# Optimization experiments

Measured on AMD Instinct MI355X. Metric: run time of the kernel, lower is better.

## Reference

```python
import jax, jax.numpy as jnp
import numpy as np

B, H, N = 2, 4, 4096


def setup_inputs() -> dict:
    key = jax.random.key(0)
    ranking = jax.random.normal(key, (B, H, N, 1), dtype=jnp.float32)
    return {"ranking": ranking}


def reference(ranking):
    b_s, h, n = ranking.shape[:3]
    r = ranking[..., 0]  # [b, h, n]
    # stable descending argsort of ranking*100 (negate; jnp stable sort keeps tie order)
    sorted_idx = jnp.argsort(-r * 100.0, axis=2, stable=True)  # [b, h, n] int
    r_sort = jnp.take_along_axis(r, sorted_idx, axis=2)
    # rel_scaler = cumsum of ones = 1..n (no mask case)
    rel_scaler = jnp.cumsum(jnp.ones_like(r_sort), axis=2)
    rel_minus = jnp.cumsum(r_sort, axis=2)
    relative_ranking = rel_minus - rel_scaler * r_sort
    rel_scaler = jnp.maximum(rel_scaler - 1.0, 0.0)  # 0..n-1
    # Hrelu forward: hard ReLU (custom backward in torch; forward math is relu)
    rank = jax.nn.relu(relative_ranking)
    indicator = rel_scaler - rank
    indicator = jnp.where(indicator < 0, indicator + n, indicator)
    perm_value = jnp.exp(-indicator * 10.0)
    # sparse COO (bh, row, col) -> coalesce == scatter-add into dense [b*h, n, n]
    rows = rel_scaler.astype(jnp.int32).reshape(b_s * h, n)
    cols = sorted_idx.reshape(b_s * h, n).astype(jnp.int32)
    vals = perm_value.reshape(b_s * h, n)
    bh = jnp.arange(b_s * h, dtype=jnp.int32)[:, None]
    perm = jnp.zeros((b_s * h, n, n), jnp.float32).at[bh, rows, cols].add(vals)
    return perm
```

## Files before the change

kernel.cpp:

```cpp
#include <hip/hip_runtime.h>
#include <math.h>
#include <float.h>

#define N 4096
#define BH 8
#define THREADS 256
#define PARTS 32
#define EPB (N / PARTS)
#define CHUNK (N / THREADS)

__device__ __forceinline__ unsigned int desc_key(float r) {
    float k = r * 100.0f;
    unsigned int b = __float_as_uint(k);
    unsigned int asc = (b & 0x80000000u) ? ~b : (b | 0x80000000u);
    return ~asc;
}

__global__ __launch_bounds__(THREADS)
void rank_kernel(const float* __restrict__ ranking,
                 int* __restrict__ cols,
                 float* __restrict__ rsort) {
    __shared__ unsigned int keys[N];
    __shared__ unsigned short partial[THREADS];

    const int bh   = blockIdx.x / PARTS;
    const int part = blockIdx.x % PARTS;
    const float* r = ranking + (size_t)bh * N;

    for (int i = threadIdx.x; i < N; i += THREADS)
        keys[i] = desc_key(r[i]);
    __syncthreads();

    const int e_local = threadIdx.x & (EPB - 1);
    const int half    = threadIdx.x >> 7;
    const int e       = part * EPB + e_local;
    const unsigned int mykey = keys[e];

    int cnt = 0;
    const uint4* k4 = (const uint4*)keys;
    const int k4_begin = half * (N / 8);
    #pragma unroll 4
    for (int k = k4_begin; k < k4_begin + N / 8; ++k) {
        uint4 kk = k4[k];
        int kb = k * 4;
        cnt += (kk.x < mykey) || (kk.x == mykey && (kb + 0) < e);
        cnt += (kk.y < mykey) || (kk.y == mykey && (kb + 1) < e);
        cnt += (kk.z < mykey) || (kk.z == mykey && (kb + 2) < e);
        cnt += (kk.w < mykey) || (kk.w == mykey && (kb + 3) < e);
    }
    partial[threadIdx.x] = (unsigned short)cnt;
    __syncthreads();

    if (half == 0) {
        int rank = cnt + (int)partial[threadIdx.x + 128];
        size_t o = (size_t)bh * N + rank;
        cols[o]  = e;
        rsort[o] = r[e];
    }
}

__global__ __launch_bounds__(THREADS)
void scan_kernel(const float* __restrict__ rsort,
                 float* __restrict__ vals) {
    __shared__ double chunk_sums[THREADS];

    const int bh  = blockIdx.x;
    const int tid = threadIdx.x;
    const float* rs = rsort + (size_t)bh * N;
    const int base = tid * CHUNK;

    float  v[CHUNK];
    double local[CHUNK];
    const float4* f4 = (const float4*)(rs + base);
    #pragma unroll
    for (int q = 0; q < CHUNK / 4; ++q) {
        float4 w = f4[q];
        v[q * 4 + 0] = w.x; v[q * 4 + 1] = w.y;
        v[q * 4 + 2] = w.z; v[q * 4 + 3] = w.w;
    }
    double s = 0.0;
    #pragma unroll
    for (int q = 0; q < CHUNK; ++q) { s += (double)v[q]; local[q] = s; }
    chunk_sums[tid] = s;
    __syncthreads();

    double off = 0.0;
    for (int t = 0; t < tid; ++t) off += chunk_sums[t];

    #pragma unroll
    for (int q = 0; q < CHUNK; ++q) {
        int i = base + q;
        double cumsum = off + local[q];
        double rel    = cumsum - (double)(i + 1) * (double)v[q];
        double rank   = rel > 0.0 ? rel : 0.0;
        double ind    = (double)i - rank;
        if (ind < 0.0) ind += (double)N;
        if (ind < 0.0) ind = 0.0;
        vals[(size_t)bh * N + i] = (float)exp(ind * -10.0);
    }
}

__global__ __launch_bounds__(THREADS)
void fill_kernel(const int* __restrict__ cols,
                 const float* __restrict__ vals,
                 float* __restrict__ out) {
    const size_t row = blockIdx.x;
    const int   c = cols[row];
    const float v = vals[row];
    float4* o = (float4*)(out + row * (size_t)N);
    const int fc  = c >> 2;
    const int tid = threadIdx.x;
    #pragma unroll
    for (int q = 0; q < 4; ++q) {
        int f = tid + THREADS * q;
        float4 w = {0.f, 0.f, 0.f, 0.f};
        if (f == fc) ((float*)&w)[c & 3] = v;
        o[f] = w;
    }
}

extern "C" void kernel_launch(void* const* d_in, const int* in_sizes, int n_in,
                              void* d_out, int out_size, void* d_ws, size_t ws_size,
                              hipStream_t stream) {
    const float* ranking = (const float*)d_in[0];
    float* out = (float*)d_out;

    int*   cols  = (int*)d_ws;
    float* rsort = (float*)((char*)d_ws + sizeof(int)   * (size_t)BH * N);
    float* vals  = (float*)((char*)d_ws + sizeof(int)*2 * (size_t)BH * N);

    rank_kernel<<<BH * PARTS, THREADS, 0, stream>>>(ranking, cols, rsort);
    scan_kernel<<<BH, THREADS, 0, stream>>>(rsort, vals);
    fill_kernel<<<BH * N, THREADS, 0, stream>>>(cols, vals, out);
}
```

Measured before the change: 585.7 us.

## Use 64-bit key+index sort keys and register-block 4 elements per thread in ranking

The rank kernel now packs the descending float key and the element index into one 64-bit key, so stable tie-breaking becomes a single unsigned comparison. Each thread ranks 4 elements against one of 8 key slices, reusing each shared-memory key load across 4 comparisons. Per-slice partial counts are summed afterwards. This cuts comparison and LDS-load work in the rank stage, but doubles shared-memory key storage to 32KB, which may lower occupancy. The rank kernel is likely a small part of total time next to the 512MB output fill.

```diff
diff --git a/kernel.cpp b/kernel.cpp
--- a/kernel.cpp
+++ b/kernel.cpp
@@ -6,53 +6,65 @@
 #define BH 8
 #define THREADS 256
 #define PARTS 32
-#define EPB (N / PARTS)
+#define EPB 128
+#define EPT 4
+#define SLICES 8
+#define KPS (N / SLICES)
 #define CHUNK (N / THREADS)
 
-__device__ __forceinline__ unsigned int desc_key(float r) {
+__device__ __forceinline__ unsigned long long desc_key64(float r, int i) {
     float k = r * 100.0f;
     unsigned int b = __float_as_uint(k);
     unsigned int asc = (b & 0x80000000u) ? ~b : (b | 0x80000000u);
-    return ~asc;
+    return ((unsigned long long)(~asc) << 32) | (unsigned int)i;
 }
 
 __global__ __launch_bounds__(THREADS)
 void rank_kernel(const float* __restrict__ ranking,
                  int* __restrict__ cols,
                  float* __restrict__ rsort) {
-    __shared__ unsigned int keys[N];
-    __shared__ unsigned short partial[THREADS];
+    __shared__ unsigned long long keys[N];
+    __shared__ unsigned short partial[SLICES * EPB];
 
     const int bh   = blockIdx.x / PARTS;
     const int part = blockIdx.x % PARTS;
     const float* r = ranking + (size_t)bh * N;
 
     for (int i = threadIdx.x; i < N; i += THREADS)
-        keys[i] = desc_key(r[i]);
+        keys[i] = desc_key64(r[i], i);
     __syncthreads();
 
-    const int e_local = threadIdx.x & (EPB - 1);
-    const int half    = threadIdx.x >> 7;
-    const int e       = part * EPB + e_local;
-    const unsigned int mykey = keys[e];
+    const int g = threadIdx.x & 31;
+    const int s = threadIdx.x >> 5;
+    const int e_base = g * EPT;
 
-    int cnt = 0;
-    const uint4* k4 = (const uint4*)keys;
-    const int k4_begin = half * (N / 8);
+    unsigned long long mykey[EPT];
+    #pragma unroll
+    for (int j = 0; j < EPT; ++j)
+        mykey[j] = keys[part * EPB + e_base + j];
+
+    int cnt0 = 0, cnt1 = 0, cnt2 = 0, cnt3 = 0;
+    const ulonglong2* k2 = (const ulonglong2*)(keys + s * KPS);
     #pragma unroll 4
-    for (int k = k4_begin; k < k4_begin + N / 8; ++k) {
-        uint4 kk = k4[k];
-        int kb = k * 4;
-        cnt += (kk.x < mykey) || (kk.x == mykey && (kb + 0) < e);
-        cnt += (kk.y < mykey) || (kk.y == mykey && (kb + 1) < e);
-        cnt += (kk.z < mykey) || (kk.z == mykey && (kb + 2) < e);
-        cnt += (kk.w < mykey) || (kk.w == mykey && (kb + 3) < e);
+    for (int k = 0; k < KPS / 2; ++k) {
+        ulonglong2 kk = k2[k];
+        cnt0 += (kk.x < mykey[0]) + (kk.y < mykey[0]);
+        cnt1 += (kk.x < mykey[1]) + (kk.y < mykey[1]);
+        cnt2 += (kk.x < mykey[2]) + (kk.y < mykey[2]);
+        cnt3 += (kk.x < mykey[3]) + (kk.y < mykey[3]);
     }
-    partial[threadIdx.x] = (unsigned short)cnt;
+    partial[s * EPB + e_base + 0] = (unsigned short)cnt0;
+    partial[s * EPB + e_base + 1] = (unsigned short)cnt1;
+    partial[s * EPB + e_base + 2] = (unsigned short)cnt2;
+    partial[s * EPB + e_base + 3] = (unsigned short)cnt3;
     __syncthreads();
 
-    if (half == 0) {
-        int rank = cnt + (int)partial[threadIdx.x + 128];
+    if (threadIdx.x < EPB) {
+        int rank = 0;
+        #pragma unroll
+        for (int t = 0; t < SLICES; ++t)
+            rank += (int)partial[t * EPB + threadIdx.x];
+        int e = part * EPB + threadIdx.x;
         size_t o = (size_t)bh * N + rank;
         cols[o]  = e;
         rsort[o] = r[e];
```

New measurement: 556.4 us. -5.0%, faster.
